# Kernel optimization log

Measured on AMD Instinct MI355X. Metric: run time of the kernel, lower is better.

Reference implementation:

```python
import jax, jax.numpy as jnp
import numpy as np


def _wn(v, g):
    # weight norm over input axis: w[:, j] = g[j] * v[:, j] / ||v[:, j]||
    norm = jnp.sqrt(jnp.sum(v * v, axis=0, keepdims=True))
    return v * (g[None, :] / norm)


def setup_inputs() -> dict:
    key = jax.random.key(0)
    ks = jax.random.split(key, 6)
    M, K1, H, OUT = 65536, 512, 1024, 512
    x = jax.random.normal(ks[0], (M, K1), dtype=jnp.float32)
    v1 = jax.random.normal(ks[1], (K1, H), dtype=jnp.float32) * 0.05
    v2 = jax.random.normal(ks[2], (H, H), dtype=jnp.float32) * 0.05
    v3 = jax.random.normal(ks[3], (H, H), dtype=jnp.float32) * 0.05
    v4 = jax.random.normal(ks[4], (H, H), dtype=jnp.float32) * 0.05
    v5 = jax.random.normal(ks[5], (H, OUT), dtype=jnp.float32) * 0.05
    g1 = jnp.ones((H,), jnp.float32)
    g2 = jnp.ones((H,), jnp.float32)
    g3 = jnp.ones((H,), jnp.float32)
    g4 = jnp.ones((H,), jnp.float32)
    g5 = jnp.ones((OUT,), jnp.float32)
    return {"x": x, "v1": v1, "g1": g1, "v2": v2, "g2": g2,
            "v3": v3, "g3": g3, "v4": v4, "g4": g4, "v5": v5, "g5": g5}


def reference(x, v1, g1, v2, g2, v3, g3, v4, g4, v5, g5):
    w1 = _wn(v1, g1)
    w2 = _wn(v2, g2)
    w3 = _wn(v3, g3)
    w4 = _wn(v4, g4)
    w5 = _wn(v5, g5)
    h1 = jax.nn.softplus(x @ w1)    # [M, H]
    h2 = jax.nn.softplus(h1 @ w2)
    h3 = jax.nn.softplus(h2 @ w3)
    h4 = jax.nn.softplus(h3 @ w4)
    out = h4 @ w5                   # final layer linear
    return out
```

## Files before the change

### kernel.cpp

```cpp
#include <hip/hip_runtime.h>
#include <hip/hip_bf16.h>
#include <cstdint>

typedef unsigned short u16;
typedef __attribute__((ext_vector_type(8))) _Float16 f16x8;
typedef __attribute__((ext_vector_type(4))) float f32x4;
typedef __attribute__((ext_vector_type(8))) unsigned short u16x8;

typedef const __attribute__((address_space(1))) void* gas1p;
typedef __attribute__((address_space(3))) void* las3p;
typedef const __attribute__((address_space(3))) u16* lc16p;

__device__ __forceinline__ void gld_lds16(const void* g, void* l) {
    __builtin_amdgcn_global_load_lds((gas1p)g, (las3p)l, 16, 0, 0);
}

template<int OFF>
__device__ __forceinline__ f16x8 dsr128o(const u16* p) {
    f16x8 r;
    asm volatile("ds_read_b128 %0, %1 offset:%2" : "=v"(r) : "v"((lc16p)p), "i"(OFF));
    return r;
}

__device__ __forceinline__ u16 f2h(float f) {
    _Float16 h = (_Float16)f;
    return __builtin_bit_cast(u16, h);
}

__global__ void cvt_x_kernel(const float4* __restrict__ x, u16* __restrict__ xb) {
    size_t i = (size_t)blockIdx.x * blockDim.x + threadIdx.x;
    float4 a = x[2 * i];
    float4 b = x[2 * i + 1];
    u16x8 o;
    o[0] = f2h(a.x); o[1] = f2h(a.y); o[2] = f2h(a.z); o[3] = f2h(a.w);
    o[4] = f2h(b.x); o[5] = f2h(b.y); o[6] = f2h(b.z); o[7] = f2h(b.w);
    *(u16x8*)&xb[i * 8] = o;
}

struct WnDesc {
    const float* v; const float* g; u16* wT; float* partial;
    int K; int N; int blk0;
};
struct WnPack { WnDesc d[5]; int nlayer; };

__global__ void wn_partial_all(WnPack p) {
    int b = blockIdx.x;
    int l = 0;
    while (l + 1 < p.nlayer && b >= p.d[l + 1].blk0) l++;
    const WnDesc& d = p.d[l];
    int lb = b - d.blk0;
    int nbx = d.N >> 6;
    int bx = lb % nbx, seg = lb / nbx;

    int lane = threadIdx.x & 63;
    int tr = threadIdx.x >> 6;
    int n = bx * 64 + lane;
    int kseg = d.K >> 3;
    int kbeg = seg * kseg;
    float s = 0.f;
    for (int k = kbeg + tr; k < kbeg + kseg; k += 4) {
        float x = d.v[(size_t)k * d.N + n];
        s += x * x;
    }
    __shared__ float red[4][64];
    red[tr][lane] = s;
    __syncthreads();
    if (tr == 0)
        d.partial[seg * d.N + n] = red[0][lane] + red[1][lane] + red[2][lane] + red[3][lane];
}

__global__ void wn_write_all(WnPack p) {
    int b = blockIdx.x;
    int l = 0;
    while (l + 1 < p.nlayer && b >= p.d[l + 1].blk0) l++;
    const WnDesc& d = p.d[l];
    int lb = b - d.blk0;
    int nbx = d.N >> 6;
    int bx = lb % nbx, seg = lb / nbx;

    int lane = threadIdx.x & 63;
    int tr = threadIdx.x >> 6;
    int n = bx * 64 + lane;
    float s = 0.f;
#pragma unroll
    for (int i = 0; i < 8; i++) s += d.partial[i * d.N + n];
    float sc = d.g[n] / sqrtf(s);

    int kseg = d.K >> 3;
    int kbeg = seg * kseg;
    for (int k = kbeg + tr; k < kbeg + kseg; k += 4)
        d.wT[(size_t)n * d.K + k] = f2h(d.v[(size_t)k * d.N + n] * sc);
}

template<int N, int K, bool ACT, bool OUTF32>
__global__ __launch_bounds__(512, 4) void gemm_mb(
    const u16* __restrict__ A, const u16* __restrict__ Bt,
    u16* __restrict__ Ch, float* __restrict__ Cf)
{
    constexpr int M = 65536;
    constexpr int NT = K / 32;
    constexpr int NTN = N / 256;
    constexpr int NWG = (M / 128) * NTN;

    __shared__ u16 sA[2][128 * 32];
    __shared__ u16 sB[2][256 * 32];

    const int bid = blockIdx.x;
    const int wk = (bid & 7) * (NWG >> 3) + (bid >> 3);
    const int tm = wk / NTN, tn = wk % NTN;
    const long m0 = (long)tm * 128;
    const int n0 = tn * 256;

    const int tid = threadIdx.x;
    const int lane = tid & 63;
    const int wid = tid >> 6;
    const int wm = (wid >> 2) * 64;
    const int wn = (wid & 3) * 64;

    const int r4 = tid >> 2;
    const int sG = ((tid & 3) - (r4 & 3)) & 3;
    const u16* Ab  = A  + (m0 + r4) * (size_t)K + sG * 8;
    const u16* Bb  = Bt + (size_t)(n0 + r4) * K + sG * 8;
    const u16* Bb2 = Bt + (size_t)(n0 + 128 + r4) * K + sG * 8;
    const int dst8 = tid * 8;

    auto stage = [&](int buf, int t) {
        gld_lds16(Ab + (size_t)t * 32, &sA[buf][dst8]);
        gld_lds16(Bb + (size_t)t * 32, &sB[buf][dst8]);
        gld_lds16(Bb2 + (size_t)t * 32, &sB[buf][4096 + dst8]);
    };

    const int lrow = lane & 15;
    const int lq = ((lane >> 4) + (lane & 3)) & 3;
    const int aoff = (wm + lrow) * 32 + lq * 8;
    const int boff = (wn + lrow) * 32 + lq * 8;

    f32x4 acc[4][4] = {};
    f16x8 a[4], b[4];

    auto BAR = [&]() { __builtin_amdgcn_s_barrier(); };
#define LGKM0 { asm volatile("s_waitcnt lgkmcnt(0)"); __builtin_amdgcn_sched_barrier(0); }
#define VMC0  { asm volatile("s_waitcnt vmcnt(0)");  __builtin_amdgcn_sched_barrier(0); }

    stage(0, 0);
    VMC0;
    BAR();

    for (int t = 0; t < NT; t++) {
        const int cur = t & 1, nxt = cur ^ 1;
        if (t + 1 < NT) stage(nxt, t + 1);

        const u16* pA = &sA[cur][aoff];
        const u16* pB = &sB[cur][boff];
        a[0] = dsr128o<0>(pA);    a[1] = dsr128o<1024>(pA);
        a[2] = dsr128o<2048>(pA); a[3] = dsr128o<3072>(pA);
        b[0] = dsr128o<0>(pB);    b[1] = dsr128o<1024>(pB);
        b[2] = dsr128o<2048>(pB); b[3] = dsr128o<3072>(pB);
        LGKM0;

        __builtin_amdgcn_s_setprio(1);
#pragma unroll
        for (int i = 0; i < 4; i++)
#pragma unroll
            for (int j = 0; j < 4; j++)
                acc[i][j] = __builtin_amdgcn_mfma_f32_16x16x32_f16(a[i], b[j], acc[i][j], 0, 0, 0);
        __builtin_amdgcn_s_setprio(0);

        if (t + 1 < NT) {
            VMC0;
            BAR();
        }
    }
#undef LGKM0
#undef VMC0

    const long crow0 = m0 + wm + ((lane >> 4) << 2);
    const int ccol0 = n0 + wn + (lane & 15);
#pragma unroll
    for (int fi = 0; fi < 4; fi++) {
#pragma unroll
        for (int r = 0; r < 4; r++) {
            const size_t rowoff = (size_t)(crow0 + fi * 16 + r) * N;
#pragma unroll
            for (int fj = 0; fj < 4; fj++) {
                float v = acc[fi][fj][r];
                if (ACT) v = fmaxf(v, 0.f) + __logf(1.f + __expf(-fabsf(v)));
                if (OUTF32) Cf[rowoff + ccol0 + fj * 16] = v;
                else        Ch[rowoff + ccol0 + fj * 16] = f2h(v);
            }
        }
    }
}

extern "C" void kernel_launch(void* const* d_in, const int* in_sizes, int n_in,
                              void* d_out, int out_size, void* d_ws, size_t ws_size,
                              hipStream_t stream) {
    const float* x  = (const float*)d_in[0];
    const float* v1 = (const float*)d_in[1];
    const float* g1 = (const float*)d_in[2];
    const float* v2 = (const float*)d_in[3];
    const float* g2 = (const float*)d_in[4];
    const float* v3 = (const float*)d_in[5];
    const float* g3 = (const float*)d_in[6];
    const float* v4 = (const float*)d_in[7];
    const float* g4 = (const float*)d_in[8];
    const float* v5 = (const float*)d_in[9];
    const float* g5 = (const float*)d_in[10];
    float* out = (float*)d_out;

    const int M = 65536;
    char* ws = (char*)d_ws;
    u16* bufA = (u16*)(ws);
    u16* bufB = (u16*)(ws + 0x8000000ULL);
    u16* w1T  = (u16*)(ws + 0x10000000ULL);
    u16* w2T  = w1T + 1024 * 512;
    u16* w3T  = w2T + 1024 * 1024;
    u16* w4T  = w3T + 1024 * 1024;
    u16* w5T  = w4T + 1024 * 1024;
    float* part = (float*)(ws + 0x10800000ULL);

    cvt_x_kernel<<<(M * 512) / (256 * 8), 256, 0, stream>>>((const float4*)x, bufB);

    WnPack pk;
    int cum = 0;
    auto mk = [&](int i, const float* v, const float* g, u16* wT, int K, int N) {
        pk.d[i] = WnDesc{v, g, wT, part + i * 8 * 1024, K, N, cum};
        cum += (N / 64) * 8;
    };
    mk(0, v1, g1, w1T, 512, 1024);
    mk(1, v2, g2, w2T, 1024, 1024);
    mk(2, v3, g3, w3T, 1024, 1024);
    mk(3, v4, g4, w4T, 1024, 1024);
    mk(4, v5, g5, w5T, 1024, 512);
    pk.nlayer = 5;

    wn_partial_all<<<cum, 256, 0, stream>>>(pk);
    wn_write_all<<<cum, 256, 0, stream>>>(pk);

    gemm_mb<1024, 512,  true,  false><<<2048, 512, 0, stream>>>(bufB, w1T, bufA, nullptr);
    gemm_mb<1024, 1024, true,  false><<<2048, 512, 0, stream>>>(bufA, w2T, bufB, nullptr);
    gemm_mb<1024, 1024, true,  false><<<2048, 512, 0, stream>>>(bufB, w3T, bufA, nullptr);
    gemm_mb<1024, 1024, true,  false><<<2048, 512, 0, stream>>>(bufA, w4T, bufB, nullptr);
    gemm_mb<512,  1024, false, true ><<<1024, 512, 0, stream>>>(bufB, w5T, nullptr, out);

    (void)in_sizes; (void)n_in; (void)out_size; (void)ws_size;
}
```

Baseline: 755.3 us.

## Switch GEMM to 32x32x16 MFMA with reswizzled LDS and split waits

```diff
diff --git a/kernel.cpp b/kernel.cpp
--- a/kernel.cpp
+++ b/kernel.cpp
@@ -5,6 +5,7 @@
 typedef unsigned short u16;
 typedef __attribute__((ext_vector_type(8))) _Float16 f16x8;
 typedef __attribute__((ext_vector_type(4))) float f32x4;
+typedef __attribute__((ext_vector_type(16))) float f32x16;
 typedef __attribute__((ext_vector_type(8))) unsigned short u16x8;
 
 typedef const __attribute__((address_space(1))) void* gas1p;
@@ -93,7 +94,7 @@
 }
 
 template<int N, int K, bool ACT, bool OUTF32>
-__global__ __launch_bounds__(512, 4) void gemm_mb(
+__global__ __launch_bounds__(512, 4) void gemm_mb2(
     const u16* __restrict__ A, const u16* __restrict__ Bt,
     u16* __restrict__ Ch, float* __restrict__ Cf)
 {
@@ -118,7 +119,7 @@
     const int wn = (wid & 3) * 64;
 
     const int r4 = tid >> 2;
-    const int sG = ((tid & 3) - (r4 & 3)) & 3;
+    const int sG = ((tid & 3) - (r4 >> 1)) & 3;
     const u16* Ab  = A  + (m0 + r4) * (size_t)K + sG * 8;
     const u16* Bb  = Bt + (size_t)(n0 + r4) * K + sG * 8;
     const u16* Bb2 = Bt + (size_t)(n0 + 128 + r4) * K + sG * 8;
@@ -130,16 +131,20 @@
         gld_lds16(Bb2 + (size_t)t * 32, &sB[buf][4096 + dst8]);
     };
 
-    const int lrow = lane & 15;
-    const int lq = ((lane >> 4) + (lane & 3)) & 3;
-    const int aoff = (wm + lrow) * 32 + lq * 8;
-    const int boff = (wn + lrow) * 32 + lq * 8;
-
-    f32x4 acc[4][4] = {};
-    f16x8 a[4], b[4];
+    const int lrow = lane & 31;
+    const int ls = lane >> 5;
+    const int q0 = (ls + (lrow >> 1)) & 3;
+    const int q1 = q0 ^ 2;
+    const int aoff0 = (wm + lrow) * 32 + q0 * 8;
+    const int aoff1 = (wm + lrow) * 32 + q1 * 8;
+    const int boff0 = (wn + lrow) * 32 + q0 * 8;
+    const int boff1 = (wn + lrow) * 32 + q1 * 8;
+
+    f32x16 acc[2][2] = {};
+    f16x8 a0[2], a1[2], b0[2], b1[2];
 
     auto BAR = [&]() { __builtin_amdgcn_s_barrier(); };
-#define LGKM0 { asm volatile("s_waitcnt lgkmcnt(0)"); __builtin_amdgcn_sched_barrier(0); }
+#define LGKM(n) { asm volatile("s_waitcnt lgkmcnt(" #n ")"); __builtin_amdgcn_sched_barrier(0); }
 #define VMC0  { asm volatile("s_waitcnt vmcnt(0)");  __builtin_amdgcn_sched_barrier(0); }
 
     stage(0, 0);
@@ -150,20 +155,30 @@
         const int cur = t & 1, nxt = cur ^ 1;
         if (t + 1 < NT) stage(nxt, t + 1);
 
-        const u16* pA = &sA[cur][aoff];
-        const u16* pB = &sB[cur][boff];
-        a[0] = dsr128o<0>(pA);    a[1] = dsr128o<1024>(pA);
-        a[2] = dsr128o<2048>(pA); a[3] = dsr128o<3072>(pA);
-        b[0] = dsr128o<0>(pB);    b[1] = dsr128o<1024>(pB);
-        b[2] = dsr128o<2048>(pB); b[3] = dsr128o<3072>(pB);
-        LGKM0;
-
+        const u16* pA0 = &sA[cur][aoff0];
+        const u16* pA1 = &sA[cur][aoff1];
+        const u16* pB0 = &sB[cur][boff0];
+        const u16* pB1 = &sB[cur][boff1];
+        a0[0] = dsr128o<0>(pA0); a0[1] = dsr128o<2048>(pA0);
+        b0[0] = dsr128o<0>(pB0); b0[1] = dsr128o<2048>(pB0);
+        a1[0] = dsr128o<0>(pA1); a1[1] = dsr128o<2048>(pA1);
+        b1[0] = dsr128o<0>(pB1); b1[1] = dsr128o<2048>(pB1);
+
+        LGKM(4);
         __builtin_amdgcn_s_setprio(1);
 #pragma unroll
-        for (int i = 0; i < 4; i++)
-#pragma unroll
-            for (int j = 0; j < 4; j++)
-                acc[i][j] = __builtin_amdgcn_mfma_f32_16x16x32_f16(a[i], b[j], acc[i][j], 0, 0, 0);
+        for (int i = 0; i < 2; i++)
+#pragma unroll
+            for (int j = 0; j < 2; j++)
+                acc[i][j] = __builtin_amdgcn_mfma_f32_32x32x16_f16(a0[i], b0[j], acc[i][j], 0, 0, 0);
+        __builtin_amdgcn_s_setprio(0);
+        LGKM(0);
+        __builtin_amdgcn_s_setprio(1);
+#pragma unroll
+        for (int i = 0; i < 2; i++)
+#pragma unroll
+            for (int j = 0; j < 2; j++)
+                acc[i][j] = __builtin_amdgcn_mfma_f32_32x32x16_f16(a1[i], b1[j], acc[i][j], 0, 0, 0);
         __builtin_amdgcn_s_setprio(0);
 
         if (t + 1 < NT) {
@@ -171,22 +186,23 @@
             BAR();
         }
     }
-#undef LGKM0
+#undef LGKM
 #undef VMC0
 
-    const long crow0 = m0 + wm + ((lane >> 4) << 2);
-    const int ccol0 = n0 + wn + (lane & 15);
-#pragma unroll
-    for (int fi = 0; fi < 4; fi++) {
-#pragma unroll
-        for (int r = 0; r < 4; r++) {
-            const size_t rowoff = (size_t)(crow0 + fi * 16 + r) * N;
-#pragma unroll
-            for (int fj = 0; fj < 4; fj++) {
-                float v = acc[fi][fj][r];
+    const long crowb = m0 + wm + 4 * (lane >> 5);
+    const int ccolb = n0 + wn + (lane & 31);
+#pragma unroll
+    for (int fi = 0; fi < 2; fi++) {
+#pragma unroll
+        for (int fj = 0; fj < 2; fj++) {
+#pragma unroll
+            for (int reg = 0; reg < 16; reg++) {
+                const long row = crowb + fi * 32 + (reg & 3) + 8 * (reg >> 2);
+                float v = acc[fi][fj][reg];
                 if (ACT) v = fmaxf(v, 0.f) + __logf(1.f + __expf(-fabsf(v)));
-                if (OUTF32) Cf[rowoff + ccol0 + fj * 16] = v;
-                else        Ch[rowoff + ccol0 + fj * 16] = f2h(v);
+                const size_t idx = (size_t)row * N + ccolb + fj * 32;
+                if (OUTF32) Cf[idx] = v;
+                else        Ch[idx] = f2h(v);
             }
         }
     }
@@ -237,11 +253,11 @@
     wn_partial_all<<<cum, 256, 0, stream>>>(pk);
     wn_write_all<<<cum, 256, 0, stream>>>(pk);
 
-    gemm_mb<1024, 512,  true,  false><<<2048, 512, 0, stream>>>(bufB, w1T, bufA, nullptr);
-    gemm_mb<1024, 1024, true,  false><<<2048, 512, 0, stream>>>(bufA, w2T, bufB, nullptr);
-    gemm_mb<1024, 1024, true,  false><<<2048, 512, 0, stream>>>(bufB, w3T, bufA, nullptr);
-    gemm_mb<1024, 1024, true,  false><<<2048, 512, 0, stream>>>(bufA, w4T, bufB, nullptr);
-    gemm_mb<512,  1024, false, true ><<<1024, 512, 0, stream>>>(bufB, w5T, nullptr, out);
+    gemm_mb2<1024, 512,  true,  false><<<2048, 512, 0, stream>>>(bufB, w1T, bufA, nullptr);
+    gemm_mb2<1024, 1024, true,  false><<<2048, 512, 0, stream>>>(bufA, w2T, bufB, nullptr);
+    gemm_mb2<1024, 1024, true,  false><<<2048, 512, 0, stream>>>(bufB, w3T, bufA, nullptr);
+    gemm_mb2<1024, 1024, true,  false><<<2048, 512, 0, stream>>>(bufA, w4T, bufB, nullptr);
+    gemm_mb2<512,  1024, false, true ><<<1024, 512, 0, stream>>>(bufB, w5T, nullptr, out);
 
     (void)in_sizes; (void)n_in; (void)out_size; (void)ws_size;
 }
```

Measured after the change: 824.7 us. 9.2% more time.

## Store activations in k-octet blocked layout and load A directly to registers

Applied to the files above, without the earlier changes.

```diff
diff --git a/kernel.cpp b/kernel.cpp
--- a/kernel.cpp
+++ b/kernel.cpp
@@ -92,101 +92,137 @@
         d.wT[(size_t)n * d.K + k] = f2h(d.v[(size_t)k * d.N + n] * sc);
 }
 
-template<int N, int K, bool ACT, bool OUTF32>
-__global__ __launch_bounds__(512, 4) void gemm_mb(
+template<int N, int K, bool ADIR, bool OUTBLK>
+__global__ __launch_bounds__(256, 4) void gemm_v14(
     const u16* __restrict__ A, const u16* __restrict__ Bt,
-    u16* __restrict__ Ch, float* __restrict__ Cf)
+    u16* __restrict__ Co, float* __restrict__ Cf)
 {
     constexpr int M = 65536;
     constexpr int NT = K / 32;
     constexpr int NTN = N / 256;
-    constexpr int NWG = (M / 128) * NTN;
-
-    __shared__ u16 sA[2][128 * 32];
-    __shared__ u16 sB[2][256 * 32];
+    constexpr int NWG = (M / 64) * NTN;
+    constexpr int LDSZ = 2 * 8192 + (ADIR ? 0 : 2 * 2048);
+
+    __shared__ u16 lds[LDSZ];
 
     const int bid = blockIdx.x;
     const int wk = (bid & 7) * (NWG >> 3) + (bid >> 3);
     const int tm = wk / NTN, tn = wk % NTN;
-    const long m0 = (long)tm * 128;
+    const long m0 = (long)tm * 64;
     const int n0 = tn * 256;
 
     const int tid = threadIdx.x;
     const int lane = tid & 63;
     const int wid = tid >> 6;
-    const int wm = (wid >> 2) * 64;
-    const int wn = (wid & 3) * 64;
-
-    const int r4 = tid >> 2;
-    const int sG = ((tid & 3) - (r4 & 3)) & 3;
-    const u16* Ab  = A  + (m0 + r4) * (size_t)K + sG * 8;
-    const u16* Bb  = Bt + (size_t)(n0 + r4) * K + sG * 8;
-    const u16* Bb2 = Bt + (size_t)(n0 + 128 + r4) * K + sG * 8;
-    const int dst8 = tid * 8;
-
-    auto stage = [&](int buf, int t) {
-        gld_lds16(Ab + (size_t)t * 32, &sA[buf][dst8]);
-        gld_lds16(Bb + (size_t)t * 32, &sB[buf][dst8]);
-        gld_lds16(Bb2 + (size_t)t * 32, &sB[buf][4096 + dst8]);
+    const int wn = wid * 64;
+
+    const int rB = tid >> 2;
+    const int gslot = (tid & 3) ^ ((rB >> 1) & 3);
+    const u16* Bsrc = Bt + (size_t)(n0 + rB) * K + gslot * 8;
+    auto stB = [&](int buf, int t) {
+#pragma unroll
+        for (int c = 0; c < 4; c++)
+            gld_lds16(Bsrc + (size_t)(64 * c) * K + (size_t)t * 32,
+                      &lds[buf * 8192 + c * 2048 + tid * 8]);
     };
 
     const int lrow = lane & 15;
-    const int lq = ((lane >> 4) + (lane & 3)) & 3;
-    const int aoff = (wm + lrow) * 32 + lq * 8;
-    const int boff = (wn + lrow) * 32 + lq * 8;
+    const int koct = lane >> 4;
+    const int swz = (koct ^ ((lrow >> 1) & 3)) * 8;
+    const int boffL = lrow * 32 + swz;
+
+    const u16* pA;
+    const u16* Asrc = nullptr;
+    int aoffL = 0;
+    if (ADIR) {
+        pA = A + ((size_t)koct * M + m0 + lrow) * 8;
+    } else {
+        const int rA = tid >> 2;
+        Asrc = A + (m0 + rA) * (size_t)K + gslot * 8;
+        aoffL = lrow * 32 + swz;
+        pA = nullptr;
+    }
+    auto stA = [&](int buf, int t) {
+        gld_lds16(Asrc + (size_t)t * 32, &lds[16384 + buf * 2048 + tid * 8]);
+    };
 
     f32x4 acc[4][4] = {};
     f16x8 a[4], b[4];
 
     auto BAR = [&]() { __builtin_amdgcn_s_barrier(); };
 #define LGKM0 { asm volatile("s_waitcnt lgkmcnt(0)"); __builtin_amdgcn_sched_barrier(0); }
-#define VMC0  { asm volatile("s_waitcnt vmcnt(0)");  __builtin_amdgcn_sched_barrier(0); }
-
-    stage(0, 0);
-    VMC0;
+#define VMC(n) { asm volatile("s_waitcnt vmcnt(" #n ")"); __builtin_amdgcn_sched_barrier(0); }
+
+    auto aload = [&](int t) {
+        const u16* p = pA + (size_t)t * (4 * (size_t)M * 8);
+#pragma unroll
+        for (int fi = 0; fi < 4; fi++)
+            a[fi] = *(const f16x8*)(p + fi * 128);
+    };
+
+    stB(0, 0);
+    if (ADIR) {
+        aload(0);
+        VMC(4);
+    } else {
+        stA(0, 0);
+        VMC(0);
+    }
     BAR();
 
     for (int t = 0; t < NT; t++) {
         const int cur = t & 1, nxt = cur ^ 1;
-        if (t + 1 < NT) stage(nxt, t + 1);
-
-        const u16* pA = &sA[cur][aoff];
-        const u16* pB = &sB[cur][boff];
-        a[0] = dsr128o<0>(pA);    a[1] = dsr128o<1024>(pA);
-        a[2] = dsr128o<2048>(pA); a[3] = dsr128o<3072>(pA);
+        const bool more = (t + 1 < NT);
+
+        const u16* pB = &lds[cur * 8192 + wn * 32 + boffL];
         b[0] = dsr128o<0>(pB);    b[1] = dsr128o<1024>(pB);
         b[2] = dsr128o<2048>(pB); b[3] = dsr128o<3072>(pB);
+        if (!ADIR) {
+            const u16* pAl = &lds[16384 + cur * 2048 + aoffL];
+            a[0] = dsr128o<0>(pAl);    a[1] = dsr128o<1024>(pAl);
+            a[2] = dsr128o<2048>(pAl); a[3] = dsr128o<3072>(pAl);
+        }
+        if (more) { stB(nxt, t + 1); if (!ADIR) stA(nxt, t + 1); }
         LGKM0;
 
         __builtin_amdgcn_s_setprio(1);
 #pragma unroll
-        for (int i = 0; i < 4; i++)
-#pragma unroll
-            for (int j = 0; j < 4; j++)
-                acc[i][j] = __builtin_amdgcn_mfma_f32_16x16x32_f16(a[i], b[j], acc[i][j], 0, 0, 0);
+        for (int fi = 0; fi < 4; fi++)
+#pragma unroll
+            for (int fj = 0; fj < 4; fj++)
+                acc[fi][fj] = __builtin_amdgcn_mfma_f32_16x16x32_f16(a[fi], b[fj], acc[fi][fj], 0, 0, 0);
         __builtin_amdgcn_s_setprio(0);
 
-        if (t + 1 < NT) {
-            VMC0;
+        if (more) {
+            if (ADIR) {
+                aload(t + 1);
+                VMC(4);
+            } else {
+                VMC(0);
+            }
             BAR();
         }
     }
 #undef LGKM0
-#undef VMC0
-
-    const long crow0 = m0 + wm + ((lane >> 4) << 2);
+#undef VMC
+
+    const long crow0 = m0 + ((lane >> 4) << 2);
     const int ccol0 = n0 + wn + (lane & 15);
 #pragma unroll
     for (int fi = 0; fi < 4; fi++) {
 #pragma unroll
         for (int r = 0; r < 4; r++) {
-            const size_t rowoff = (size_t)(crow0 + fi * 16 + r) * N;
+            const long m = crow0 + fi * 16 + r;
 #pragma unroll
             for (int fj = 0; fj < 4; fj++) {
                 float v = acc[fi][fj][r];
-                if (ACT) v = fmaxf(v, 0.f) + __logf(1.f + __expf(-fabsf(v)));
-                if (OUTF32) Cf[rowoff + ccol0 + fj * 16] = v;
-                else        Ch[rowoff + ccol0 + fj * 16] = f2h(v);
+                if (OUTBLK) {
+                    v = fmaxf(v, 0.f) + __logf(1.f + __expf(-fabsf(v)));
+                    const int n = ccol0 + fj * 16;
+                    Co[((size_t)(n >> 3) * M + m) * 8 + (n & 7)] = f2h(v);
+                } else {
+                    Cf[(size_t)m * N + ccol0 + fj * 16] = v;
+                }
             }
         }
     }
@@ -237,11 +273,11 @@
     wn_partial_all<<<cum, 256, 0, stream>>>(pk);
     wn_write_all<<<cum, 256, 0, stream>>>(pk);
 
-    gemm_mb<1024, 512,  true,  false><<<2048, 512, 0, stream>>>(bufB, w1T, bufA, nullptr);
-    gemm_mb<1024, 1024, true,  false><<<2048, 512, 0, stream>>>(bufA, w2T, bufB, nullptr);
-    gemm_mb<1024, 1024, true,  false><<<2048, 512, 0, stream>>>(bufB, w3T, bufA, nullptr);
-    gemm_mb<1024, 1024, true,  false><<<2048, 512, 0, stream>>>(bufA, w4T, bufB, nullptr);
-    gemm_mb<512,  1024, false, true ><<<1024, 512, 0, stream>>>(bufB, w5T, nullptr, out);
+    gemm_v14<1024, 512,  false, true ><<<4096, 256, 0, stream>>>(bufB, w1T, bufA, nullptr);
+    gemm_v14<1024, 1024, true,  true ><<<4096, 256, 0, stream>>>(bufA, w2T, bufB, nullptr);
+    gemm_v14<1024, 1024, true,  true ><<<4096, 256, 0, stream>>>(bufB, w3T, bufA, nullptr);
+    gemm_v14<1024, 1024, true,  true ><<<4096, 256, 0, stream>>>(bufA, w4T, bufB, nullptr);
+    gemm_v14<512,  1024, true,  false><<<2048, 256, 0, stream>>>(bufB, w5T, nullptr, out);
 
     (void)in_sizes; (void)n_in; (void)out_size; (void)ws_size;
 }
```

Result: slower. 939.3 us (+24.4%).
